# Kernel tuning notes

Hardware: AMD Instinct MI355X
Metric: run time of the kernel (lower is better)

Reference implementation:

```python
import jax, jax.numpy as jnp
import numpy as np

N_NODES = 100_000
N_EDGES = 1_600_000
D_IN, D_HID, D_OUT = 256, 64, 32
NUM_PROP = 10
ALPHA = 0.1


def setup_inputs() -> dict:
    key = jax.random.key(0)
    ks = jax.random.split(key, 8)
    features = jax.random.normal(ks[0], (N_NODES, D_IN), dtype=jnp.float32)
    row = jax.random.randint(ks[1], (N_EDGES,), 0, N_NODES, dtype=jnp.int32)
    col = jax.random.randint(ks[2], (N_EDGES,), 0, N_NODES, dtype=jnp.int32)
    # positive edge weights (stand-in for symmetric-normalized adjacency values)
    edge_vals = jax.random.uniform(ks[3], (N_EDGES,), dtype=jnp.float32) / 16.0
    W1 = jax.random.normal(ks[4], (D_IN, D_HID), dtype=jnp.float32) / np.sqrt(D_IN)
    b1 = jnp.zeros((D_HID,), dtype=jnp.float32)
    W2 = jax.random.normal(ks[5], (D_HID, D_OUT), dtype=jnp.float32) / np.sqrt(D_HID)
    b2 = jnp.zeros((D_OUT,), dtype=jnp.float32)
    return {"features": features, "row": row, "col": col, "edge_vals": edge_vals,
            "W1": W1, "b1": b1, "W2": W2, "b2": b2}


def _spmm(row, col, vals, x):
    # COO sparse-dense matmul: out[r] += vals[e] * x[col[e]] for each edge e
    return jax.ops.segment_sum(vals[:, None] * x[col], row, num_segments=N_NODES)


def reference(features, row, col, edge_vals, W1, b1, W2, b2):
    # head_transform: 2-layer MLP
    x = jax.nn.relu(features @ W1 + b1) @ W2 + b2  # [N, D_OUT]
    x0 = x
    # APPNP propagation: x = (1-alpha) * (A @ x) + alpha * x0
    def body(_, x):
        return (1.0 - ALPHA) * _spmm(row, col, edge_vals, x) + ALPHA * x0
    x = jax.lax.fori_loop(0, NUM_PROP, body, x)
    return x
```

## Files before the change

kernel.cpp:

```cpp
#include <hip/hip_runtime.h>

#define N_NODES 100000
#define N_EDGES 1600000
#define D_IN    256
#define D_HID   64
#define D_OUT   32
#define NPROP   10

#define NBUCK 196
#define CHUNK 6080
#define NCHUNK ((N_EDGES + CHUNK - 1) / CHUNK)

typedef _Float16 half_t;
typedef _Float16 h8  __attribute__((ext_vector_type(8)));
typedef _Float16 h4  __attribute__((ext_vector_type(4)));
typedef float    f4v __attribute__((ext_vector_type(4)));

__global__ __launch_bounds__(256) void pack_kernel(
    const float* __restrict__ W1, const float* __restrict__ W2,
    half_t* __restrict__ W1T, half_t* __restrict__ W2T)
{
  int t = blockIdx.x * 256 + threadIdx.x;
  if (t < 64 * 256) { int n = t >> 8, k = t & 255; W1T[t] = (half_t)W1[k * 64 + n]; }
  if (t < 32 * 64)  { int n = t >> 6, k = t & 63;  W2T[t] = (half_t)W2[k * 32 + n]; }
}

#define HSTRIDE 72

__global__ __launch_bounds__(256, 2) void mlp_kernel(
    const float* __restrict__ F, const half_t* __restrict__ W1T,
    const float* __restrict__ b1, const half_t* __restrict__ W2T,
    const float* __restrict__ b2, half_t* __restrict__ x0h)
{
  __shared__ half_t h_lds[4 * 16 * HSTRIDE];
  __shared__ half_t out_lds[4 * 16 * 32];
  int t = threadIdx.x;
  int w = t >> 6, lane = t & 63;
  int m = lane & 15, q = lane >> 4;
  int gw = blockIdx.x * 4 + w;
  int node0 = gw * 16;
  if (node0 > N_NODES - 16) node0 = N_NODES - 16;

  const float* ap = F + (size_t)(node0 + m) * D_IN + q * 8;
  float4 fr[16];
#pragma unroll
  for (int s = 0; s < 8; ++s) {
    fr[2 * s]     = *(const float4*)(ap + s * 32);
    fr[2 * s + 1] = *(const float4*)(ap + s * 32 + 4);
  }

  h8 af[8];
#pragma unroll
  for (int s = 0; s < 8; ++s) {
    float4 f0 = fr[2 * s], f1 = fr[2 * s + 1];
    h8 a;
    a[0] = (_Float16)f0.x; a[1] = (_Float16)f0.y;
    a[2] = (_Float16)f0.z; a[3] = (_Float16)f0.w;
    a[4] = (_Float16)f1.x; a[5] = (_Float16)f1.y;
    a[6] = (_Float16)f1.z; a[7] = (_Float16)f1.w;
    af[s] = a;
  }

  f4v acc[4];
#pragma unroll
  for (int i = 0; i < 4; ++i) acc[i] = (f4v){0.f, 0.f, 0.f, 0.f};
  const half_t* bp = W1T + (size_t)m * D_IN + q * 8;
#pragma unroll
  for (int s = 0; s < 8; ++s) {
    h8 b0 = *(const h8*)(bp + 0 * 16 * D_IN + s * 32);
    h8 b1v = *(const h8*)(bp + 1 * 16 * D_IN + s * 32);
    h8 b2v = *(const h8*)(bp + 2 * 16 * D_IN + s * 32);
    h8 b3v = *(const h8*)(bp + 3 * 16 * D_IN + s * 32);
    acc[0] = __builtin_amdgcn_mfma_f32_16x16x32_f16(af[s], b0, acc[0], 0, 0, 0);
    acc[1] = __builtin_amdgcn_mfma_f32_16x16x32_f16(af[s], b1v, acc[1], 0, 0, 0);
    acc[2] = __builtin_amdgcn_mfma_f32_16x16x32_f16(af[s], b2v, acc[2], 0, 0, 0);
    acc[3] = __builtin_amdgcn_mfma_f32_16x16x32_f16(af[s], b3v, acc[3], 0, 0, 0);
  }

  half_t* hw = h_lds + w * 16 * HSTRIDE;
#pragma unroll
  for (int ht = 0; ht < 4; ++ht) {
    float bb = b1[ht * 16 + m];
#pragma unroll
    for (int i = 0; i < 4; ++i) {
      float hv = fmaxf(acc[ht][i] + bb, 0.f);
      hw[(q * 4 + i) * HSTRIDE + ht * 16 + m] = (half_t)hv;
    }
  }
  __syncthreads();

  f4v o0 = {0.f, 0.f, 0.f, 0.f}, o1 = {0.f, 0.f, 0.f, 0.f};
#pragma unroll
  for (int s = 0; s < 2; ++s) {
    h8 a = *(const h8*)(hw + m * HSTRIDE + s * 32 + q * 8);
    h8 bb0 = *(const h8*)(W2T + (size_t)m * D_HID + s * 32 + q * 8);
    h8 bb1 = *(const h8*)(W2T + (size_t)(16 + m) * D_HID + s * 32 + q * 8);
    o0 = __builtin_amdgcn_mfma_f32_16x16x32_f16(a, bb0, o0, 0, 0, 0);
    o1 = __builtin_amdgcn_mfma_f32_16x16x32_f16(a, bb1, o1, 0, 0, 0);
  }
  half_t* ow = out_lds + w * 16 * 32;
  {
    float c0 = b2[m], c1 = b2[16 + m];
#pragma unroll
    for (int i = 0; i < 4; ++i) {
      ow[(q * 4 + i) * 32 + m]      = (half_t)(o0[i] + c0);
      ow[(q * 4 + i) * 32 + 16 + m] = (half_t)(o1[i] + c1);
    }
  }
  __syncthreads();

  {
    int nl = lane >> 2, qq = lane & 3;
    *(int4*)(x0h + (size_t)(node0 + nl) * D_OUT + qq * 8) =
        *(const int4*)(ow + nl * 32 + qq * 8);
  }
}

__global__ __launch_bounds__(256) void bhist_kernel(
    const int* __restrict__ row, int* __restrict__ bcnt)
{
  __shared__ int lb[NBUCK];
  int t = threadIdx.x;
  for (int i = t; i < NBUCK; i += 256) lb[i] = 0;
  __syncthreads();
  int stride = gridDim.x * 256;
  for (int e = blockIdx.x * 256 + t; e < N_EDGES; e += stride)
    atomicAdd(&lb[row[e] >> 9], 1);
  __syncthreads();
  for (int i = t; i < NBUCK; i += 256)
    if (lb[i]) atomicAdd(&bcnt[i], lb[i]);
}

__global__ __launch_bounds__(256) void bscan_kernel(
    const int* __restrict__ bcnt, int* __restrict__ bbase, int* __restrict__ pbase)
{
  __shared__ int l1[256], l2[256];
  int t = threadIdx.x;
  int a = (t < NBUCK) ? bcnt[t] : 0;
  int r = (t < NBUCK) ? (((a + 3) & ~3) + 3 * 512) : 0;
  l1[t] = a; l2[t] = r;
  __syncthreads();
  for (int off = 1; off < 256; off <<= 1) {
    int x1 = (t >= off) ? l1[t - off] : 0;
    int x2 = (t >= off) ? l2[t - off] : 0;
    __syncthreads();
    l1[t] += x1; l2[t] += x2;
    __syncthreads();
  }
  if (t < NBUCK) { bbase[t] = l1[t] - a; pbase[t] = l2[t] - r; }
  if (t == NBUCK - 1) { bbase[NBUCK] = l1[t]; pbase[NBUCK] = l2[t]; }
}

__global__ __launch_bounds__(256) void bscatter_kernel(
    const int* __restrict__ row, const int* __restrict__ col,
    const float* __restrict__ vals, int* __restrict__ bfill,
    const int* __restrict__ bbase, int2* __restrict__ ebuck)
{
  __shared__ int2 img[CHUNK];
  __shared__ unsigned short sbk[CHUNK];
  __shared__ int cnt[NBUCK], base[NBUCK], gb[NBUCK], fil[NBUCK];
  __shared__ int ssc[256];
  int t = threadIdx.x;
  int e0 = blockIdx.x * CHUNK;
  int n = min(CHUNK, N_EDGES - e0);

  for (int i = t; i < NBUCK; i += 256) { cnt[i] = 0; fil[i] = 0; }
  __syncthreads();
  for (int i = t; i < n; i += 256) atomicAdd(&cnt[row[e0 + i] >> 9], 1);
  __syncthreads();
  int c = (t < NBUCK) ? cnt[t] : 0;
  ssc[t] = c;
  __syncthreads();
  for (int off = 1; off < 256; off <<= 1) {
    int add = (t >= off) ? ssc[t - off] : 0;
    __syncthreads();
    ssc[t] += add;
    __syncthreads();
  }
  if (t < NBUCK) {
    base[t] = ssc[t] - c;
    gb[t] = c ? atomicAdd(&bfill[t], c) : 0;
  }
  __syncthreads();
  for (int i = t; i < n; i += 256) {
    int r = row[e0 + i];
    int bk = r >> 9;
    int p = base[bk] + atomicAdd(&fil[bk], 1);
    img[p] = make_int2(col[e0 + i] | ((r & 511) << 17),
                       __float_as_int(vals[e0 + i]));
    sbk[p] = (unsigned short)bk;
  }
  __syncthreads();
  for (int i = t; i < n; i += 256) {
    int bk = sbk[i];
    ebuck[bbase[bk] + gb[bk] + (i - base[bk])] = img[i];
  }
}

__global__ __launch_bounds__(256) void bsort_kernel(
    const int* __restrict__ bbase, const int* __restrict__ pbase,
    const int2* __restrict__ ebuck, int2* __restrict__ epack,
    int* __restrict__ row_ptr)
{
  __shared__ int acnt[512], loff[513], lfill[512], ssc[256];
  int b = blockIdx.x, t = threadIdx.x;
  int r0 = b * 512;
  int nr = min(512, N_NODES - r0);
  int eb = bbase[b];
  int ne = bbase[b + 1] - eb;
  int pb = pbase[b];

  acnt[t] = 0; acnt[t + 256] = 0;
  lfill[t] = 0; lfill[t + 256] = 0;
  __syncthreads();
  for (int i = t; i < ne; i += 256)
    atomicAdd(&acnt[((unsigned)ebuck[eb + i].x) >> 17], 1);
  __syncthreads();
  int i0 = 2 * t, i1 = 2 * t + 1;
  int a0 = acnt[i0], a1 = acnt[i1];
  int p0 = (a0 + 3) & ~3, p1 = (a1 + 3) & ~3;
  int s = p0 + p1;
  ssc[t] = s;
  __syncthreads();
  for (int off = 1; off < 256; off <<= 1) {
    int add = (t >= off) ? ssc[t - off] : 0;
    __syncthreads();
    ssc[t] += add;
    __syncthreads();
  }
  int ex = ssc[t] - s;
  loff[i0] = ex;
  loff[i1] = ex + p0;
  if (t == 255) loff[512] = ssc[255];
  __syncthreads();
  int T = ssc[255];
  int slack = (pbase[b + 1] - pb) - T;
  int units = min(slack >> 2, nr);
  if (i0 < nr) row_ptr[r0 + i0] = pb + loff[i0] + 4 * min(i0, units);
  if (i1 < nr) row_ptr[r0 + i1] = pb + loff[i1] + 4 * min(i1, units);
  if (b == NBUCK - 1 && t == 0)
    row_ptr[N_NODES] = pb + loff[nr] + 4 * units;
  __syncthreads();
  for (int i = t; i < ne; i += 256) {
    int2 ed = ebuck[eb + i];
    int lr = ((unsigned)ed.x) >> 17;
    int cl = ed.x & 0x1FFFF;
    int p = loff[lr] + 4 * min(lr, units) + atomicAdd(&lfill[lr], 1);
    epack[pb + p] = make_int2(cl, ed.y);
  }
  __syncthreads();
  for (int i = t; i < nr; i += 256) {
    int a = acnt[i];
    int size_i = ((a + 3) & ~3) + 4 * (i < units);
    int st = loff[i] + 4 * min(i, units);
    for (int p = st + a; p < st + size_i; ++p)
      epack[pb + p] = make_int2(0, 0);
  }
}

__global__ __launch_bounds__(256) void spmm_kernel(
    const int* __restrict__ rp, const int2* __restrict__ ep,
    const half_t* __restrict__ xin, const half_t* __restrict__ x0h,
    half_t* __restrict__ xout, float* __restrict__ fout, int last)
{
  int gt = blockIdx.x * 256 + threadIdx.x;
  int r = gt >> 3;
  int c4 = (gt & 7) * 4;
  if (r >= N_NODES) return;
  int e0 = rp[r], e1 = rp[r + 1];

  float acc[4] = {0.f, 0.f, 0.f, 0.f};
  for (int e = e0; e < e1; e += 4) {
    int2 p0 = ep[e];
    int2 p1 = ep[e + 1];
    int2 p2 = ep[e + 2];
    int2 p3 = ep[e + 3];
    h4 g0 = *(const h4*)(xin + (size_t)p0.x * D_OUT + c4);
    h4 g1 = *(const h4*)(xin + (size_t)p1.x * D_OUT + c4);
    h4 g2 = *(const h4*)(xin + (size_t)p2.x * D_OUT + c4);
    h4 g3 = *(const h4*)(xin + (size_t)p3.x * D_OUT + c4);
    float v0 = __int_as_float(p0.y);
    float v1 = __int_as_float(p1.y);
    float v2 = __int_as_float(p2.y);
    float v3 = __int_as_float(p3.y);
#pragma unroll
    for (int j = 0; j < 4; ++j) {
      acc[j] = fmaf(v0, (float)g0[j], acc[j]);
      acc[j] = fmaf(v1, (float)g1[j], acc[j]);
      acc[j] = fmaf(v2, (float)g2[j], acc[j]);
      acc[j] = fmaf(v3, (float)g3[j], acc[j]);
    }
  }

  h4 x0v = *(const h4*)(x0h + (size_t)r * D_OUT + c4);
  if (last) {
    float4 o;
    o.x = 0.9f * acc[0] + 0.1f * (float)x0v[0];
    o.y = 0.9f * acc[1] + 0.1f * (float)x0v[1];
    o.z = 0.9f * acc[2] + 0.1f * (float)x0v[2];
    o.w = 0.9f * acc[3] + 0.1f * (float)x0v[3];
    *(float4*)(fout + (size_t)r * D_OUT + c4) = o;
  } else {
    h4 o;
#pragma unroll
    for (int j = 0; j < 4; ++j)
      o[j] = (half_t)(0.9f * acc[j] + 0.1f * (float)x0v[j]);
    *(h4*)(xout + (size_t)r * D_OUT + c4) = o;
  }
}

extern "C" void kernel_launch(void* const* d_in, const int* in_sizes, int n_in,
                              void* d_out, int out_size, void* d_ws, size_t ws_size,
                              hipStream_t stream) {
  const float* F     = (const float*)d_in[0];
  const int*   row   = (const int*)  d_in[1];
  const int*   col   = (const int*)  d_in[2];
  const float* evals = (const float*)d_in[3];
  const float* W1    = (const float*)d_in[4];
  const float* b1    = (const float*)d_in[5];
  const float* W2    = (const float*)d_in[6];
  const float* b2    = (const float*)d_in[7];
  float* out = (float*)d_out;

  char* w = (char*)d_ws;
  half_t* x0h    = (half_t*)(w);
  half_t* P      = (half_t*)(w +  6400000);
  half_t* Q      = (half_t*)(w + 12800000);
  int2*   ebuck  = (int2*)  (w +  6400000);
  int2*   epack  = (int2*)  (w + 19200000);
  int*   row_ptr = (int*)   (w + 34600192);
  int*   bcnt    = (int*)   (w + 35000576);
  int*   bfill   = (int*)   (w + 35001600);
  int*   bbase   = (int*)   (w + 35002624);
  int*   pbase   = (int*)   (w + 35003648);
  half_t* W1T    = (half_t*)(w + 35004672);
  half_t* W2T    = (half_t*)(w + 35037440);

  pack_kernel<<<64, 256, 0, stream>>>(W1, W2, W1T, W2T);
  mlp_kernel<<<(N_NODES / 16 + 3) / 4, 256, 0, stream>>>(F, W1T, b1, W2T, b2, x0h);

  hipMemsetAsync(bcnt, 0, 2048, stream);
  bhist_kernel<<<640, 256, 0, stream>>>(row, bcnt);
  bscan_kernel<<<1, 256, 0, stream>>>(bcnt, bbase, pbase);
  bscatter_kernel<<<NCHUNK, 256, 0, stream>>>(row, col, evals, bfill, bbase, ebuck);
  bsort_kernel<<<NBUCK, 256, 0, stream>>>(bbase, pbase, ebuck, epack, row_ptr);

  const int grid_spmm = (N_NODES * 8 + 255) / 256;
  for (int i = 0; i < NPROP; ++i) {
    const half_t* xin = (i == 0) ? x0h : ((i & 1) ? P : Q);
    half_t* xout = (i & 1) ? Q : P;
    int last = (i == NPROP - 1);
    spmm_kernel<<<grid_spmm, 256, 0, stream>>>(
        row_ptr, epack, xin, x0h, xout, out, last);
  }
}
```

Before: 531.6 us.

## Fuse MLP blocks into graph-build kernels and grid-stride the SpMM

Splits the MLP head into three slices of blocks and packs each slice into the same launch as a graph-preprocessing stage: histogram plus weight pack, scan, bucket scatter, and bucket sort. The two independent workloads can then share the GPU and fewer kernels are launched. SpMM now runs a fixed 2048-block grid with a grid-stride loop instead of one thread per row-quarter. The merged kernels carry the larger of the two LDS footprints and a launch bound of two blocks, which may lower occupancy for the scatter and sort stages.

New measurement: 521.1 us. -2.0%, faster.

```diff
diff --git a/kernel.cpp b/kernel.cpp
--- a/kernel.cpp
+++ b/kernel.cpp
@@ -11,33 +11,32 @@
 #define CHUNK 6080
 #define NCHUNK ((N_EDGES + CHUNK - 1) / CHUNK)
 
+#define MLP_BLOCKS 1563
+#define MLP_A 700
+#define MLP_B 500
+#define MLP_C (MLP_BLOCKS - MLP_A - MLP_B)
+
+#define SPMM_BLOCKS 2048
+
 typedef _Float16 half_t;
 typedef _Float16 h8  __attribute__((ext_vector_type(8)));
 typedef _Float16 h4  __attribute__((ext_vector_type(4)));
 typedef float    f4v __attribute__((ext_vector_type(4)));
 
-__global__ __launch_bounds__(256) void pack_kernel(
-    const float* __restrict__ W1, const float* __restrict__ W2,
-    half_t* __restrict__ W1T, half_t* __restrict__ W2T)
-{
-  int t = blockIdx.x * 256 + threadIdx.x;
-  if (t < 64 * 256) { int n = t >> 8, k = t & 255; W1T[t] = (half_t)W1[k * 64 + n]; }
-  if (t < 32 * 64)  { int n = t >> 6, k = t & 63;  W2T[t] = (half_t)W2[k * 32 + n]; }
-}
-
 #define HSTRIDE 72
-
-__global__ __launch_bounds__(256, 2) void mlp_kernel(
+#define MLP_LDS_BYTES (4 * 16 * HSTRIDE * 2 + 4 * 16 * 32 * 2)
+
+static __device__ __forceinline__ void mlp_body(
+    int mb, int t, char* smem,
     const float* __restrict__ F, const half_t* __restrict__ W1T,
     const float* __restrict__ b1, const half_t* __restrict__ W2T,
     const float* __restrict__ b2, half_t* __restrict__ x0h)
 {
-  __shared__ half_t h_lds[4 * 16 * HSTRIDE];
-  __shared__ half_t out_lds[4 * 16 * 32];
-  int t = threadIdx.x;
+  half_t* h_lds   = (half_t*)smem;
+  half_t* out_lds = (half_t*)(smem + 4 * 16 * HSTRIDE * 2);
   int w = t >> 6, lane = t & 63;
   int m = lane & 15, q = lane >> 4;
-  int gw = blockIdx.x * 4 + w;
+  int gw = mb * 4 + w;
   int node0 = gw * 16;
   if (node0 > N_NODES - 16) node0 = N_NODES - 16;
 
@@ -116,145 +115,180 @@
   }
 }
 
-__global__ __launch_bounds__(256) void bhist_kernel(
-    const int* __restrict__ row, int* __restrict__ bcnt)
+__global__ __launch_bounds__(256) void mix0_kernel(
+    const int* __restrict__ row, int* __restrict__ bcnt,
+    const float* __restrict__ W1, const float* __restrict__ W2,
+    half_t* __restrict__ W1T, half_t* __restrict__ W2T)
 {
   __shared__ int lb[NBUCK];
-  int t = threadIdx.x;
-  for (int i = t; i < NBUCK; i += 256) lb[i] = 0;
-  __syncthreads();
-  int stride = gridDim.x * 256;
-  for (int e = blockIdx.x * 256 + t; e < N_EDGES; e += stride)
-    atomicAdd(&lb[row[e] >> 9], 1);
-  __syncthreads();
-  for (int i = t; i < NBUCK; i += 256)
-    if (lb[i]) atomicAdd(&bcnt[i], lb[i]);
-}
-
-__global__ __launch_bounds__(256) void bscan_kernel(
-    const int* __restrict__ bcnt, int* __restrict__ bbase, int* __restrict__ pbase)
-{
-  __shared__ int l1[256], l2[256];
-  int t = threadIdx.x;
-  int a = (t < NBUCK) ? bcnt[t] : 0;
-  int r = (t < NBUCK) ? (((a + 3) & ~3) + 3 * 512) : 0;
-  l1[t] = a; l2[t] = r;
-  __syncthreads();
-  for (int off = 1; off < 256; off <<= 1) {
-    int x1 = (t >= off) ? l1[t - off] : 0;
-    int x2 = (t >= off) ? l2[t - off] : 0;
-    __syncthreads();
-    l1[t] += x1; l2[t] += x2;
-    __syncthreads();
-  }
-  if (t < NBUCK) { bbase[t] = l1[t] - a; pbase[t] = l2[t] - r; }
-  if (t == NBUCK - 1) { bbase[NBUCK] = l1[t]; pbase[NBUCK] = l2[t]; }
-}
-
-__global__ __launch_bounds__(256) void bscatter_kernel(
+  int b = blockIdx.x, t = threadIdx.x;
+  if (b < 640) {
+    for (int i = t; i < NBUCK; i += 256) lb[i] = 0;
+    __syncthreads();
+    const int stride = 640 * 256;
+    for (int e = b * 256 + t; e < N_EDGES; e += stride)
+      atomicAdd(&lb[row[e] >> 9], 1);
+    __syncthreads();
+    for (int i = t; i < NBUCK; i += 256)
+      if (lb[i]) atomicAdd(&bcnt[i], lb[i]);
+  } else {
+    int g = (b - 640) * 256 + t;
+    if (g < 64 * 256) { int n = g >> 8, k = g & 255; W1T[g] = (half_t)W1[k * 64 + n]; }
+    if (g < 32 * 64)  { int n = g >> 6, k = g & 63;  W2T[g] = (half_t)W2[k * 32 + n]; }
+  }
+}
+
+__global__ __launch_bounds__(256, 2) void mix1_kernel(
+    const int* __restrict__ bcnt, int* __restrict__ bbase, int* __restrict__ pbase,
+    const float* __restrict__ F, const half_t* __restrict__ W1T,
+    const float* __restrict__ b1, const half_t* __restrict__ W2T,
+    const float* __restrict__ b2, half_t* __restrict__ x0h)
+{
+  __shared__ __align__(16) char smem[MLP_LDS_BYTES];
+  int b = blockIdx.x, t = threadIdx.x;
+  if (b == 0) {
+    int* l1 = (int*)smem;
+    int* l2 = (int*)smem + 256;
+    int a = (t < NBUCK) ? bcnt[t] : 0;
+    int r = (t < NBUCK) ? (((a + 3) & ~3) + 3 * 512) : 0;
+    l1[t] = a; l2[t] = r;
+    __syncthreads();
+    for (int off = 1; off < 256; off <<= 1) {
+      int x1 = (t >= off) ? l1[t - off] : 0;
+      int x2 = (t >= off) ? l2[t - off] : 0;
+      __syncthreads();
+      l1[t] += x1; l2[t] += x2;
+      __syncthreads();
+    }
+    if (t < NBUCK) { bbase[t] = l1[t] - a; pbase[t] = l2[t] - r; }
+    if (t == NBUCK - 1) { bbase[NBUCK] = l1[t]; pbase[NBUCK] = l2[t]; }
+  } else {
+    mlp_body(b - 1, t, smem, F, W1T, b1, W2T, b2, x0h);
+  }
+}
+
+__global__ __launch_bounds__(256, 2) void mix2_kernel(
     const int* __restrict__ row, const int* __restrict__ col,
     const float* __restrict__ vals, int* __restrict__ bfill,
-    const int* __restrict__ bbase, int2* __restrict__ ebuck)
+    const int* __restrict__ bbase, int2* __restrict__ ebuck,
+    const float* __restrict__ F, const half_t* __restrict__ W1T,
+    const float* __restrict__ b1, const half_t* __restrict__ W2T,
+    const float* __restrict__ b2, half_t* __restrict__ x0h)
 {
   __shared__ int2 img[CHUNK];
   __shared__ unsigned short sbk[CHUNK];
   __shared__ int cnt[NBUCK], base[NBUCK], gb[NBUCK], fil[NBUCK];
   __shared__ int ssc[256];
-  int t = threadIdx.x;
-  int e0 = blockIdx.x * CHUNK;
-  int n = min(CHUNK, N_EDGES - e0);
-
-  for (int i = t; i < NBUCK; i += 256) { cnt[i] = 0; fil[i] = 0; }
-  __syncthreads();
-  for (int i = t; i < n; i += 256) atomicAdd(&cnt[row[e0 + i] >> 9], 1);
-  __syncthreads();
-  int c = (t < NBUCK) ? cnt[t] : 0;
-  ssc[t] = c;
-  __syncthreads();
-  for (int off = 1; off < 256; off <<= 1) {
-    int add = (t >= off) ? ssc[t - off] : 0;
-    __syncthreads();
-    ssc[t] += add;
-    __syncthreads();
-  }
-  if (t < NBUCK) {
-    base[t] = ssc[t] - c;
-    gb[t] = c ? atomicAdd(&bfill[t], c) : 0;
-  }
-  __syncthreads();
-  for (int i = t; i < n; i += 256) {
-    int r = row[e0 + i];
-    int bk = r >> 9;
-    int p = base[bk] + atomicAdd(&fil[bk], 1);
-    img[p] = make_int2(col[e0 + i] | ((r & 511) << 17),
-                       __float_as_int(vals[e0 + i]));
-    sbk[p] = (unsigned short)bk;
-  }
-  __syncthreads();
-  for (int i = t; i < n; i += 256) {
-    int bk = sbk[i];
-    ebuck[bbase[bk] + gb[bk] + (i - base[bk])] = img[i];
-  }
-}
-
-__global__ __launch_bounds__(256) void bsort_kernel(
+  __shared__ __align__(16) char smem[MLP_LDS_BYTES];
+  int b = blockIdx.x, t = threadIdx.x;
+
+  if (b < NCHUNK) {
+    int e0 = b * CHUNK;
+    int n = min(CHUNK, N_EDGES - e0);
+
+    for (int i = t; i < NBUCK; i += 256) { cnt[i] = 0; fil[i] = 0; }
+    __syncthreads();
+    for (int i = t; i < n; i += 256) atomicAdd(&cnt[row[e0 + i] >> 9], 1);
+    __syncthreads();
+    int c = (t < NBUCK) ? cnt[t] : 0;
+    ssc[t] = c;
+    __syncthreads();
+    for (int off = 1; off < 256; off <<= 1) {
+      int add = (t >= off) ? ssc[t - off] : 0;
+      __syncthreads();
+      ssc[t] += add;
+      __syncthreads();
+    }
+    if (t < NBUCK) {
+      base[t] = ssc[t] - c;
+      gb[t] = c ? atomicAdd(&bfill[t], c) : 0;
+    }
+    __syncthreads();
+    for (int i = t; i < n; i += 256) {
+      int r = row[e0 + i];
+      int bk = r >> 9;
+      int p = base[bk] + atomicAdd(&fil[bk], 1);
+      img[p] = make_int2(col[e0 + i] | ((r & 511) << 17),
+                         __float_as_int(vals[e0 + i]));
+      sbk[p] = (unsigned short)bk;
+    }
+    __syncthreads();
+    for (int i = t; i < n; i += 256) {
+      int bk = sbk[i];
+      ebuck[bbase[bk] + gb[bk] + (i - base[bk])] = img[i];
+    }
+  } else {
+    mlp_body(MLP_A + (b - NCHUNK), t, smem, F, W1T, b1, W2T, b2, x0h);
+  }
+}
+
+__global__ __launch_bounds__(256, 2) void mix3_kernel(
     const int* __restrict__ bbase, const int* __restrict__ pbase,
     const int2* __restrict__ ebuck, int2* __restrict__ epack,
-    int* __restrict__ row_ptr)
+    int* __restrict__ row_ptr,
+    const float* __restrict__ F, const half_t* __restrict__ W1T,
+    const float* __restrict__ b1, const half_t* __restrict__ W2T,
+    const float* __restrict__ b2, half_t* __restrict__ x0h)
 {
   __shared__ int acnt[512], loff[513], lfill[512], ssc[256];
+  __shared__ __align__(16) char smem[MLP_LDS_BYTES];
   int b = blockIdx.x, t = threadIdx.x;
-  int r0 = b * 512;
-  int nr = min(512, N_NODES - r0);
-  int eb = bbase[b];
-  int ne = bbase[b + 1] - eb;
-  int pb = pbase[b];
-
-  acnt[t] = 0; acnt[t + 256] = 0;
-  lfill[t] = 0; lfill[t + 256] = 0;
-  __syncthreads();
-  for (int i = t; i < ne; i += 256)
-    atomicAdd(&acnt[((unsigned)ebuck[eb + i].x) >> 17], 1);
-  __syncthreads();
-  int i0 = 2 * t, i1 = 2 * t + 1;
-  int a0 = acnt[i0], a1 = acnt[i1];
-  int p0 = (a0 + 3) & ~3, p1 = (a1 + 3) & ~3;
-  int s = p0 + p1;
-  ssc[t] = s;
-  __syncthreads();
-  for (int off = 1; off < 256; off <<= 1) {
-    int add = (t >= off) ? ssc[t - off] : 0;
-    __syncthreads();
-    ssc[t] += add;
-    __syncthreads();
-  }
-  int ex = ssc[t] - s;
-  loff[i0] = ex;
-  loff[i1] = ex + p0;
-  if (t == 255) loff[512] = ssc[255];
-  __syncthreads();
-  int T = ssc[255];
-  int slack = (pbase[b + 1] - pb) - T;
-  int units = min(slack >> 2, nr);
-  if (i0 < nr) row_ptr[r0 + i0] = pb + loff[i0] + 4 * min(i0, units);
-  if (i1 < nr) row_ptr[r0 + i1] = pb + loff[i1] + 4 * min(i1, units);
-  if (b == NBUCK - 1 && t == 0)
-    row_ptr[N_NODES] = pb + loff[nr] + 4 * units;
-  __syncthreads();
-  for (int i = t; i < ne; i += 256) {
-    int2 ed = ebuck[eb + i];
-    int lr = ((unsigned)ed.x) >> 17;
-    int cl = ed.x & 0x1FFFF;
-    int p = loff[lr] + 4 * min(lr, units) + atomicAdd(&lfill[lr], 1);
-    epack[pb + p] = make_int2(cl, ed.y);
-  }
-  __syncthreads();
-  for (int i = t; i < nr; i += 256) {
-    int a = acnt[i];
-    int size_i = ((a + 3) & ~3) + 4 * (i < units);
-    int st = loff[i] + 4 * min(i, units);
-    for (int p = st + a; p < st + size_i; ++p)
-      epack[pb + p] = make_int2(0, 0);
+
+  if (b < NBUCK) {
+    int r0 = b * 512;
+    int nr = min(512, N_NODES - r0);
+    int eb = bbase[b];
+    int ne = bbase[b + 1] - eb;
+    int pb = pbase[b];
+
+    acnt[t] = 0; acnt[t + 256] = 0;
+    lfill[t] = 0; lfill[t + 256] = 0;
+    __syncthreads();
+    for (int i = t; i < ne; i += 256)
+      atomicAdd(&acnt[((unsigned)ebuck[eb + i].x) >> 17], 1);
+    __syncthreads();
+    int i0 = 2 * t, i1 = 2 * t + 1;
+    int a0 = acnt[i0], a1 = acnt[i1];
+    int p0 = (a0 + 3) & ~3, p1 = (a1 + 3) & ~3;
+    int s = p0 + p1;
+    ssc[t] = s;
+    __syncthreads();
+    for (int off = 1; off < 256; off <<= 1) {
+      int add = (t >= off) ? ssc[t - off] : 0;
+      __syncthreads();
+      ssc[t] += add;
+      __syncthreads();
+    }
+    int ex = ssc[t] - s;
+    loff[i0] = ex;
+    loff[i1] = ex + p0;
+    if (t == 255) loff[512] = ssc[255];
+    __syncthreads();
+    int T = ssc[255];
+    int slack = (pbase[b + 1] - pb) - T;
+    int units = min(slack >> 2, nr);
+    if (i0 < nr) row_ptr[r0 + i0] = pb + loff[i0] + 4 * min(i0, units);
+    if (i1 < nr) row_ptr[r0 + i1] = pb + loff[i1] + 4 * min(i1, units);
+    if (b == NBUCK - 1 && t == 0)
+      row_ptr[N_NODES] = pb + loff[nr] + 4 * units;
+    __syncthreads();
+    for (int i = t; i < ne; i += 256) {
+      int2 ed = ebuck[eb + i];
+      int lr = ((unsigned)ed.x) >> 17;
+      int cl = ed.x & 0x1FFFF;
+      int p = loff[lr] + 4 * min(lr, units) + atomicAdd(&lfill[lr], 1);
+      epack[pb + p] = make_int2(cl, ed.y);
+    }
+    __syncthreads();
+    for (int i = t; i < nr; i += 256) {
+      int a = acnt[i];
+      int size_i = ((a + 3) & ~3) + 4 * (i < units);
+      int st = loff[i] + 4 * min(i, units);
+      for (int p = st + a; p < st + size_i; ++p)
+        epack[pb + p] = make_int2(0, 0);
+    }
+  } else {
+    mlp_body(MLP_A + MLP_B + (b - NBUCK), t, smem, F, W1T, b1, W2T, b2, x0h);
   }
 }
 
@@ -264,48 +298,50 @@
     half_t* __restrict__ xout, float* __restrict__ fout, int last)
 {
   int gt = blockIdx.x * 256 + threadIdx.x;
-  int r = gt >> 3;
-  int c4 = (gt & 7) * 4;
-  if (r >= N_NODES) return;
-  int e0 = rp[r], e1 = rp[r + 1];
-
-  float acc[4] = {0.f, 0.f, 0.f, 0.f};
-  for (int e = e0; e < e1; e += 4) {
-    int2 p0 = ep[e];
-    int2 p1 = ep[e + 1];
-    int2 p2 = ep[e + 2];
-    int2 p3 = ep[e + 3];
-    h4 g0 = *(const h4*)(xin + (size_t)p0.x * D_OUT + c4);
-    h4 g1 = *(const h4*)(xin + (size_t)p1.x * D_OUT + c4);
-    h4 g2 = *(const h4*)(xin + (size_t)p2.x * D_OUT + c4);
-    h4 g3 = *(const h4*)(xin + (size_t)p3.x * D_OUT + c4);
-    float v0 = __int_as_float(p0.y);
-    float v1 = __int_as_float(p1.y);
-    float v2 = __int_as_float(p2.y);
-    float v3 = __int_as_float(p3.y);
-#pragma unroll
-    for (int j = 0; j < 4; ++j) {
-      acc[j] = fmaf(v0, (float)g0[j], acc[j]);
-      acc[j] = fmaf(v1, (float)g1[j], acc[j]);
-      acc[j] = fmaf(v2, (float)g2[j], acc[j]);
-      acc[j] = fmaf(v3, (float)g3[j], acc[j]);
-    }
-  }
-
-  h4 x0v = *(const h4*)(x0h + (size_t)r * D_OUT + c4);
-  if (last) {
-    float4 o;
-    o.x = 0.9f * acc[0] + 0.1f * (float)x0v[0];
-    o.y = 0.9f * acc[1] + 0.1f * (float)x0v[1];
-    o.z = 0.9f * acc[2] + 0.1f * (float)x0v[2];
-    o.w = 0.9f * acc[3] + 0.1f * (float)x0v[3];
-    *(float4*)(fout + (size_t)r * D_OUT + c4) = o;
-  } else {
-    h4 o;
-#pragma unroll
-    for (int j = 0; j < 4; ++j)
-      o[j] = (half_t)(0.9f * acc[j] + 0.1f * (float)x0v[j]);
-    *(h4*)(xout + (size_t)r * D_OUT + c4) = o;
+  const int stride = SPMM_BLOCKS * 256;
+  for (int u = gt; u < N_NODES * 8; u += stride) {
+    int r = u >> 3;
+    int c4 = (u & 7) * 4;
+    int e0 = rp[r], e1 = rp[r + 1];
+
+    float acc[4] = {0.f, 0.f, 0.f, 0.f};
+    for (int e = e0; e < e1; e += 4) {
+      int2 p0 = ep[e];
+      int2 p1 = ep[e + 1];
+      int2 p2 = ep[e + 2];
+      int2 p3 = ep[e + 3];
+      h4 g0 = *(const h4*)(xin + (size_t)p0.x * D_OUT + c4);
+      h4 g1 = *(const h4*)(xin + (size_t)p1.x * D_OUT + c4);
+      h4 g2 = *(const h4*)(xin + (size_t)p2.x * D_OUT + c4);
+      h4 g3 = *(const h4*)(xin + (size_t)p3.x * D_OUT + c4);
+      float v0 = __int_as_float(p0.y);
+      float v1 = __int_as_float(p1.y);
+      float v2 = __int_as_float(p2.y);
+      float v3 = __int_as_float(p3.y);
+#pragma unroll
+      for (int j = 0; j < 4; ++j) {
+        acc[j] = fmaf(v0, (float)g0[j], acc[j]);
+        acc[j] = fmaf(v1, (float)g1[j], acc[j]);
+        acc[j] = fmaf(v2, (float)g2[j], acc[j]);
+        acc[j] = fmaf(v3, (float)g3[j], acc[j]);
+      }
+    }
+
+    h4 x0v = *(const h4*)(x0h + (size_t)r * D_OUT + c4);
+    if (last) {
+      float4 o;
+      o.x = 0.9f * acc[0] + 0.1f * (float)x0v[0];
+      o.y = 0.9f * acc[1] + 0.1f * (float)x0v[1];
+      o.z = 0.9f * acc[2] + 0.1f * (float)x0v[2];
+      o.w = 0.9f * acc[3] + 0.1f * (float)x0v[3];
+      *(float4*)(fout + (size_t)r * D_OUT + c4) = o;
+    } else {
+      h4 o;
+#pragma unroll
+      for (int j = 0; j < 4; ++j)
+        o[j] = (half_t)(0.9f * acc[j] + 0.1f * (float)x0v[j]);
+      *(h4*)(xout + (size_t)r * D_OUT + c4) = o;
+    }
   }
 }
 
@@ -336,21 +372,21 @@
   half_t* W1T    = (half_t*)(w + 35004672);
   half_t* W2T    = (half_t*)(w + 35037440);
 
-  pack_kernel<<<64, 256, 0, stream>>>(W1, W2, W1T, W2T);
-  mlp_kernel<<<(N_NODES / 16 + 3) / 4, 256, 0, stream>>>(F, W1T, b1, W2T, b2, x0h);
-
   hipMemsetAsync(bcnt, 0, 2048, stream);
-  bhist_kernel<<<640, 256, 0, stream>>>(row, bcnt);
-  bscan_kernel<<<1, 256, 0, stream>>>(bcnt, bbase, pbase);
-  bscatter_kernel<<<NCHUNK, 256, 0, stream>>>(row, col, evals, bfill, bbase, ebuck);
-  bsort_kernel<<<NBUCK, 256, 0, stream>>>(bbase, pbase, ebuck, epack, row_ptr);
-
-  const int grid_spmm = (N_NODES * 8 + 255) / 256;
+  mix0_kernel<<<640 + 64, 256, 0, stream>>>(row, bcnt, W1, W2, W1T, W2T);
+
+  mix1_kernel<<<1 + MLP_A, 256, 0, stream>>>(
+      bcnt, bbase, pbase, F, W1T, b1, W2T, b2, x0h);
+  mix2_kernel<<<NCHUNK + MLP_B, 256, 0, stream>>>(
+      row, col, evals, bfill, bbase, ebuck, F, W1T, b1, W2T, b2, x0h);
+  mix3_kernel<<<NBUCK + MLP_C, 256, 0, stream>>>(
+      bbase, pbase, ebuck, epack, row_ptr, F, W1T, b1, W2T, b2, x0h);
+
   for (int i = 0; i < NPROP; ++i) {
     const half_t* xin = (i == 0) ? x0h : ((i & 1) ? P : Q);
     half_t* xout = (i & 1) ? Q : P;
     int last = (i == NPROP - 1);
-    spmm_kernel<<<grid_spmm, 256, 0, stream>>>(
+    spmm_kernel<<<SPMM_BLOCKS, 256, 0, stream>>>(
         row_ptr, epack, xin, x0h, xout, out, last);
   }
 }
```
